# Optimization experiments

Measured on AMD Instinct MI355X. Metric: run time of the kernel, lower is better.

The kernel has to match this reference:

```python
import jax, jax.numpy as jnp
from jax import lax
import numpy as np

A = 9                 # 3 scales x 3 ratios
PRE_NMS_TOPN = 4000
POST_NMS_TOPN = 2000
NMS_THRESH = 0.7
MIN_SIZE = 16.0       # min_size * im_scale (im_info scale = 1)
NEG_INF = -1e9


def generate_anchors(base_size=16, ratios=(0.5, 1.0, 2.0), scales=(8, 16, 32)):
    ratios = np.array(ratios, dtype=np.float64)
    scales = np.array(scales, dtype=np.float64)
    w = h = float(base_size)
    xc = yc = 0.5 * (base_size - 1)
    size = w * h
    ws_r = np.round(np.sqrt(size / ratios))          # [3]
    hs_r = np.round(ws_r * ratios)                   # [3]
    ws = (ws_r[:, None] * scales[None, :]).reshape(-1)   # [9]
    hs = (hs_r[:, None] * scales[None, :]).reshape(-1)   # [9]
    anchors = np.stack([xc - 0.5 * (ws - 1), yc - 0.5 * (hs - 1),
                        xc + 0.5 * (ws - 1), yc + 0.5 * (hs - 1)], axis=1)
    return anchors.astype(np.float32)                # [9,4]


def _conv(x, w, b, padding):
    y = lax.conv_general_dilated(x, w, (1, 1), padding,
                                 dimension_numbers=('NCHW', 'OIHW', 'NCHW'))
    return y + b[None, :, None, None]


def _bbox_transform_inv(anchors, deltas):
    w = anchors[:, 2] - anchors[:, 0] + 1.0
    h = anchors[:, 3] - anchors[:, 1] + 1.0
    cx = anchors[:, 0] + 0.5 * w
    cy = anchors[:, 1] + 0.5 * h
    pcx = deltas[:, 0] * w + cx
    pcy = deltas[:, 1] * h + cy
    pw = jnp.exp(deltas[:, 2]) * w
    ph = jnp.exp(deltas[:, 3]) * h
    return jnp.stack([pcx - 0.5 * pw, pcy - 0.5 * ph,
                      pcx + 0.5 * pw, pcy + 0.5 * ph], axis=1)


def _greedy_nms(boxes, keep_init, thresh):
    # boxes already sorted by descending score; keep_init masks invalid rows
    x1, y1, x2, y2 = boxes[:, 0], boxes[:, 1], boxes[:, 2], boxes[:, 3]
    areas = (x2 - x1 + 1.0) * (y2 - y1 + 1.0)
    xx1 = jnp.maximum(x1[:, None], x1[None, :])
    yy1 = jnp.maximum(y1[:, None], y1[None, :])
    xx2 = jnp.minimum(x2[:, None], x2[None, :])
    yy2 = jnp.minimum(y2[:, None], y2[None, :])
    inter = jnp.maximum(0.0, xx2 - xx1 + 1.0) * jnp.maximum(0.0, yy2 - yy1 + 1.0)
    iou = inter / (areas[:, None] + areas[None, :] - inter)   # [N,N]
    n = boxes.shape[0]
    idx = jnp.arange(n)

    def body(i, keep):
        suppress = keep[i] & (iou[i] > thresh) & (idx > i)
        return keep & ~suppress

    return lax.fori_loop(0, n, body, keep_init)


def reference(im, feats, w_conv, b_conv, w_cls, b_cls, w_reg, b_reg):
    im_h, im_w = im.shape[2], im.shape[3]
    fh, fw = feats.shape[2], feats.shape[3]
    stride = round(im_w / fw)

    # RPN head (classifier)
    hid = jax.nn.relu(_conv(feats, w_conv, b_conv, 'SAME'))
    rpn_map = _conv(hid, w_cls, b_cls, 'SAME')       # [1, 2A, fh, fw]
    rpn_bbox = _conv(hid, w_reg, b_reg, 'SAME')      # [1, 4A, fh, fw]

    # anchor generation: [K*A, 4], shift-major / anchor-minor
    base = jnp.asarray(generate_anchors())
    sx = jnp.arange(fw, dtype=jnp.float32) * stride
    sy = jnp.arange(fh, dtype=jnp.float32) * stride
    sxx, syy = jnp.meshgrid(sx, sy)                  # [fh, fw]
    shifts = jnp.stack([sxx.ravel(), syy.ravel(), sxx.ravel(), syy.ravel()], 1)
    anchors = (base[None, :, :] + shifts[:, None, :]).reshape(-1, 4)

    # predictions, flattened in (h, w, a) order to match anchors
    deltas = rpn_bbox.transpose(0, 2, 3, 1).reshape(-1, 4)
    scores = rpn_map[:, A:, :, :].transpose(0, 2, 3, 1).reshape(-1)

    proposals = _bbox_transform_inv(anchors, deltas)
    # clip_boxes to image
    proposals = jnp.stack([
        jnp.clip(proposals[:, 0], 0.0, im_w - 1.0),
        jnp.clip(proposals[:, 1], 0.0, im_h - 1.0),
        jnp.clip(proposals[:, 2], 0.0, im_w - 1.0),
        jnp.clip(proposals[:, 3], 0.0, im_h - 1.0)], axis=1)

    # filter_boxes (min_size) expressed as a score mask (jit-friendly)
    ws = proposals[:, 2] - proposals[:, 0] + 1.0
    hs = proposals[:, 3] - proposals[:, 1] + 1.0
    valid = (ws >= MIN_SIZE) & (hs >= MIN_SIZE)
    masked_scores = jnp.where(valid, scores, NEG_INF)

    # sort descending, take pre_nms_topN
    order = jnp.argsort(-masked_scores)[:PRE_NMS_TOPN]
    top_boxes = proposals[order]
    top_scores = masked_scores[order]
    keep_init = top_scores > NEG_INF / 2

    keep = _greedy_nms(top_boxes, keep_init, NMS_THRESH)

    # take first post_nms_topN kept (already in score order), padded with zeros
    rank = jnp.cumsum(keep) - 1
    take = keep & (rank < POST_NMS_TOPN)
    dst = jnp.where(take, rank, 0)
    out_boxes = jnp.zeros((POST_NMS_TOPN, 4), dtype=top_boxes.dtype)
    out_boxes = out_boxes.at[dst].add(jnp.where(take[:, None], top_boxes, 0.0))
    out_scores = jnp.zeros((POST_NMS_TOPN, 1), dtype=top_scores.dtype)
    out_scores = out_scores.at[dst].add(jnp.where(take[:, None], top_scores[:, None], 0.0))
    return out_boxes, out_scores


def setup_inputs() -> dict:
    key = jax.random.key(0)
    ks = jax.random.split(key, 8)
    # small weight scale keeps exp(dw) in a sane range, as a trained RPN would
    return {
        'im': jax.random.normal(ks[0], (1, 3, 800, 1216), jnp.float32),
        'feats': jax.random.normal(ks[1], (1, 1024, 50, 76), jnp.float32),
        'w_conv': jax.random.normal(ks[2], (512, 1024, 3, 3), jnp.float32) * 0.001,
        'b_conv': jnp.zeros((512,), jnp.float32),
        'w_cls': jax.random.normal(ks[3], (18, 512, 1, 1), jnp.float32) * 0.01,
        'b_cls': jnp.zeros((18,), jnp.float32),
        'w_reg': jax.random.normal(ks[4], (36, 512, 1, 1), jnp.float32) * 0.01,
        'b_reg': jnp.zeros((36,), jnp.float32),
    }
```

## Files before the change

### kernel.cpp

```cpp
#include <hip/hip_runtime.h>
#include <stdint.h>
#include <math.h>

typedef unsigned long long u64;
typedef unsigned int u32;

#define CIN     1024
#define COUT    512
#define FH      50
#define FW      76
#define QP      80
#define HIDP    4096
#define FPITCH  4160
#define NPOS    3800
#define NA      34200
#define PRE_N   4000
#define POST_N  2000
#define MASKW   63
#define TBN     4032
#define KSLICES 8
#define CPS     128
#define QT      256

#define P0 (3*CIN*FPITCH)
#define P2 (512*48)
#define P3 65536

__device__ __forceinline__ void async16(const float* g, float* l) {
  __builtin_amdgcn_global_load_lds(
      (__attribute__((address_space(1))) void*)(g),
      (__attribute__((address_space(3))) void*)(l), 16, 0, 0);
}

__global__ void k_prep(const float* __restrict__ feats,
                       const float* __restrict__ w_cls, const float* __restrict__ b_cls,
                       const float* __restrict__ w_reg, const float* __restrict__ b_reg,
                       float* __restrict__ fpad3, float* __restrict__ wT, float* __restrict__ bT,
                       u32* __restrict__ hist, u32* __restrict__ ctrl,
                       double4* __restrict__ tb, float* __restrict__ ts) {
  int idx = blockIdx.x * 256 + threadIdx.x;
  if (idx < P0) {
    int tc = idx / (CIN * FPITCH);
    int rem = idx - tc * (CIN * FPITCH);
    int cin = rem / FPITCH;
    int j = rem - cin * FPITCH + tc;
    float v = 0.f;
    if (j < FPITCH) {
      int r = j / QP, u = j - r * QP;
      if (r >= 1 && r <= FH && u >= 1 && u <= FW)
        v = feats[cin * (FH * FW) + (r - 1) * FW + (u - 1)];
    }
    fpad3[idx] = v;
    return;
  }
  idx -= P0;
  if (idx < P2) {
    int c = idx / 48, o = idx - c * 48;
    float v = 0.f;
    if (o < 9) v = w_cls[(size_t)(9 + o) * 512 + c];
    else if (o < 45) v = w_reg[(size_t)(o - 9) * 512 + c];
    wT[idx] = v;
    return;
  }
  idx -= P2;
  if (idx < P3) {
    hist[idx] = 0;
    if (idx < 8) ctrl[idx] = 0;
    if (idx < 48) bT[idx] = (idx < 9) ? b_cls[9 + idx] : (idx < 45 ? b_reg[idx - 9] : 0.f);
    if (idx >= PRE_N && idx < TBN) { tb[idx] = make_double4(0.0, 0.0, 0.0, 0.0); ts[idx] = -1.0e9f; }
  }
}

__global__ void k_wt(const float* __restrict__ w, float* __restrict__ wt) {
  __shared__ float t[64][65];
  int k0 = blockIdx.x * 64, oc0 = blockIdx.y * 64;
  int tx = threadIdx.x & 63, tg = threadIdx.x >> 6;
#pragma unroll
  for (int rr = 0; rr < 16; rr++) {
    int row = tg * 16 + rr;
    t[row][tx] = w[(size_t)(oc0 + row) * 9216 + k0 + tx];
  }
  __syncthreads();
#pragma unroll
  for (int rr = 0; rr < 16; rr++) {
    int kr = tg * 16 + rr;
    wt[(size_t)(k0 + kr) * 512 + oc0 + tx] = t[tx][kr];
  }
}

__global__ __launch_bounds__(256, 4) void k_conv(const float* __restrict__ fpad3,
                                                 const float* __restrict__ wt,
                                                 float* __restrict__ hidp) {
  __shared__ __align__(16) float Bl[2][9][QT];
  const int tid = threadIdx.x;
  const int lane = tid & 63;
  const int wv = __builtin_amdgcn_readfirstlane(tid >> 6);
  const int q0 = blockIdx.x * QT;
  const int ws = (blockIdx.y << 2) + wv;
  const int c0 = blockIdx.z * CPS;

  const int rA = wv;
  const int rB = wv + 4;
  u32 offA = (u32)(rA % 3) * (CIN * FPITCH) + (u32)(rA / 3) * QP + q0 + lane * 4;
  u32 offB = (u32)(rB % 3) * (CIN * FPITCH) + (u32)(rB / 3) * QP + q0 + lane * 4;
  u32 offC = 2u * (CIN * FPITCH) + 2u * QP + q0 + lane * 4;

  float acc32[8][4];
  double acc64[8][4];
#pragma unroll
  for (int i = 0; i < 8; i++)
#pragma unroll
    for (int j = 0; j < 4; j++) { acc32[i][j] = 0.f; acc64[i][j] = 0.0; }

#define STAGE(buf, s)  do {                                                     \
    const float* _b = fpad3 + (size_t)(c0 + (s)) * FPITCH;                      \
    async16(_b + offA, &Bl[buf][rA][0]);                                        \
    async16(_b + offB, &Bl[buf][rB][0]);                                        \
    if (wv == 0) async16(_b + offC, &Bl[buf][8][0]);                            \
  } while (0)

  STAGE(0, 0);

#pragma unroll 1
  for (int s = 0; s < CPS; s++) {
    __syncthreads();
    if (s + 1 < CPS) STAGE((s + 1) & 1, s + 1);
    const float* wp = wt + ((size_t)(c0 + s) * 9 << 9) + (ws << 3);
    const int buf = s & 1;
#pragma unroll
    for (int ks = 0; ks < 9; ks++) {
      float4 b4 = *(const float4*)&Bl[buf][ks][lane * 4];
      const float* w8 = wp + (ks << 9);
#pragma unroll
      for (int i = 0; i < 8; i++) {
        float w = w8[i];
        acc32[i][0] = fmaf(w, b4.x, acc32[i][0]);
        acc32[i][1] = fmaf(w, b4.y, acc32[i][1]);
        acc32[i][2] = fmaf(w, b4.z, acc32[i][2]);
        acc32[i][3] = fmaf(w, b4.w, acc32[i][3]);
      }
    }
    if ((s & 7) == 7) {
#pragma unroll
      for (int i = 0; i < 8; i++)
#pragma unroll
        for (int j = 0; j < 4; j++) { acc64[i][j] += (double)acc32[i][j]; acc32[i][j] = 0.f; }
    }
  }
#undef STAGE

#pragma unroll
  for (int i = 0; i < 8; i++) {
    float4 o;
    o.x = (float)acc64[i][0];
    o.y = (float)acc64[i][1];
    o.z = (float)acc64[i][2];
    o.w = (float)acc64[i][3];
    *(float4*)&hidp[((size_t)(blockIdx.z * COUT + (ws << 3) + i) << 12) + q0 + lane * 4] = o;
  }
}

__global__ void k_reduce(const float* __restrict__ hidp, const float* __restrict__ bconv,
                         float* __restrict__ hid) {
  int idx = blockIdx.x * 256 + threadIdx.x;
  int oc = idx >> 12;
  double s = 0.0;
#pragma unroll
  for (int z = 0; z < KSLICES; z++)
    s += (double)hidp[idx + ((size_t)z << 21)];
  s += (double)bconv[oc];
  hid[idx] = s > 0.0 ? (float)s : 0.f;
}

__global__ __launch_bounds__(256, 8) void k_head(const float* __restrict__ hid,
                                                 const float* __restrict__ wT,
                                                 const float* __restrict__ bT,
                                                 float* __restrict__ scoresb,
                                                 float* __restrict__ deltab) {
  int lane = threadIdx.x & 63;
  int wv = threadIdx.x >> 6;
  int q = blockIdx.x * 64 + lane;
  int og = blockIdx.y * 12 + wv * 3;
  double acc0 = 0.0, acc1 = 0.0, acc2 = 0.0;
#pragma unroll 4
  for (int c = 0; c < 512; c++) {
    double hv = (double)hid[((size_t)c << 12) + q];
    const float* wr = wT + c * 48 + og;
    acc0 += hv * (double)wr[0];
    acc1 += hv * (double)wr[1];
    acc2 += hv * (double)wr[2];
  }
  int y = q / QP, x = q - y * QP;
  if (x < FW && y < FH) {
    int pos = y * FW + x;
    double a[3] = {acc0, acc1, acc2};
#pragma unroll
    for (int j = 0; j < 3; j++) {
      int o = og + j;
      float r = (float)(a[j] + (double)bT[o]);
      if (o < 9)       scoresb[o * NPOS + pos] = r;
      else if (o < 45) deltab[(o - 9) * NPOS + pos] = r;
    }
  }
}

__device__ __constant__ float AW[9] = {184.f, 368.f, 736.f, 128.f, 256.f, 512.f, 88.f, 176.f, 352.f};
__device__ __constant__ float AH[9] = {96.f, 192.f, 384.f, 128.f, 256.f, 512.f, 176.f, 352.f, 704.f};

__global__ void k_prop(const float* __restrict__ scoresb, const float* __restrict__ deltab,
                       double4* __restrict__ boxesd, u64* __restrict__ keys,
                       float* __restrict__ smask, u32* __restrict__ hist,
                       float* __restrict__ dout) {
  int g = blockIdx.x * 256 + threadIdx.x;
  if (g < 10000) dout[g] = 0.f;
  if (g >= NA) return;
  int pos = g / 9, a = g - pos * 9;
  int y = pos / FW, x = pos - y * FW;
  double w = (double)AW[a], h = (double)AH[a];
  double cx = x * 16.0 + 8.0, cy = y * 16.0 + 8.0;
  double d0 = (double)deltab[(4 * a + 0) * NPOS + pos];
  double d1 = (double)deltab[(4 * a + 1) * NPOS + pos];
  double d2 = (double)deltab[(4 * a + 2) * NPOS + pos];
  double d3 = (double)deltab[(4 * a + 3) * NPOS + pos];
  double pcx = d0 * w + cx, pcy = d1 * h + cy;
  double pw = exp(d2) * w, ph = exp(d3) * h;
  double px1 = fmin(fmax(pcx - 0.5 * pw, 0.0), 1215.0);
  double py1 = fmin(fmax(pcy - 0.5 * ph, 0.0), 799.0);
  double px2 = fmin(fmax(pcx + 0.5 * pw, 0.0), 1215.0);
  double py2 = fmin(fmax(pcy + 0.5 * ph, 0.0), 799.0);
  bool valid = (px2 - px1 + 1.0 >= 16.0) && (py2 - py1 + 1.0 >= 16.0);
  float sc = scoresb[a * NPOS + pos];
  float ms = valid ? sc : -1.0e9f;
  boxesd[g] = make_double4(px1, py1, px2, py2);
  smask[g] = ms;
  u32 u = __float_as_uint(ms);
  u = (u >> 31) ? ~u : (u | 0x80000000u);
  keys[g] = ((u64)u << 32) | (u32)(~(u32)g);
  atomicAdd(&hist[u >> 16], 1u);
}

__global__ void k_scan(const u32* __restrict__ hist, u32* __restrict__ ctrl) {
  __shared__ u32 cs[256];
  __shared__ u32 sfx[256];
  int t = threadIdx.x;
  u32 s = 0;
  for (int i = 0; i < 256; i++) s += hist[t * 256 + i];
  cs[t] = s;
  __syncthreads();
  if (t == 0) {
    u32 c = 0;
    for (int i = 255; i >= 0; i--) { sfx[i] = c; c += cs[i]; }
  }
  __syncthreads();
  u32 before = sfx[t];
  u32 c = 0;
  for (int b = 255; b >= 0; b--) {
    u32 hv = hist[t * 256 + b];
    if (before + c < PRE_N && before + c + hv >= PRE_N) {
      ctrl[0] = (u32)(t * 256 + b);
      ctrl[1] = before + c;
    }
    c += hv;
  }
}

__global__ void k_compact(const u64* __restrict__ keys, u32* __restrict__ ctrl,
                          u64* __restrict__ candK, u32* __restrict__ candG) {
  int g = blockIdx.x * 256 + threadIdx.x;
  if (g >= NA) return;
  u32 binB = ctrl[0];
  u64 k = keys[g];
  if ((u32)(k >> 48) >= binB) {
    u32 idx = atomicAdd(&ctrl[2], 1u);
    candK[idx] = k;
    candG[idx] = g;
  }
}

__global__ void k_rank(const u64* __restrict__ candK, const u32* __restrict__ candG,
                       const u32* __restrict__ ctrl, const double4* __restrict__ boxesd,
                       const float* __restrict__ smask, double4* __restrict__ tb,
                       float* __restrict__ ts) {
  __shared__ u64 kk[256];
  u32 m = ctrl[2];
  if (blockIdx.x * 256 >= m) return;
  int i = blockIdx.x * 256 + threadIdx.x;
  u64 my = (i < (int)m) ? candK[i] : 0ULL;
  u32 rank = 0;
  for (u32 base = 0; base < m; base += 256) {
    u32 j = base + threadIdx.x;
    kk[threadIdx.x] = (j < m) ? candK[j] : 0ULL;
    __syncthreads();
    u32 lim = m - base; if (lim > 256) lim = 256;
    for (u32 tt = 0; tt < lim; tt++) rank += (kk[tt] > my) ? 1u : 0u;
    __syncthreads();
  }
  if (i < (int)m && rank < PRE_N) {
    u32 g = candG[i];
    tb[rank] = boxesd[g];
    ts[rank] = smask[g];
  }
}

__global__ void k_mask(const double4* __restrict__ tb, u64* __restrict__ mask) {
  __shared__ double4 bx[64];
  int w = blockIdx.x;
  int i = blockIdx.y * 256 + threadIdx.x;
  if (threadIdx.x < 64) bx[threadIdx.x] = tb[w * 64 + threadIdx.x];
  __syncthreads();
  if (i >= PRE_N) return;
  double4 b = tb[i];
  double ai = (b.z - b.x + 1.0) * (b.w - b.y + 1.0);
  u64 word = 0;
#pragma unroll 8
  for (int j = 0; j < 64; j++) {
    int jg = w * 64 + j;
    double4 cc = bx[j];
    double xx1 = fmax(b.x, cc.x), yy1 = fmax(b.y, cc.y);
    double xx2 = fmin(b.z, cc.z), yy2 = fmin(b.w, cc.w);
    double iw = xx2 - xx1 + 1.0, ih = yy2 - yy1 + 1.0;
    iw = iw > 0.0 ? iw : 0.0; ih = ih > 0.0 ? ih : 0.0;
    double inter = iw * ih;
    double aj = (cc.z - cc.x + 1.0) * (cc.w - cc.y + 1.0);
    bool sup = (jg > i) && (inter > 0.7 * (ai + aj - inter));
    word |= sup ? (1ULL << j) : 0ULL;
  }
  mask[(size_t)i * MASKW + w] = word;
}

__global__ __launch_bounds__(64, 1) void k_nms(const u64* __restrict__ mask,
                                               const float* __restrict__ ts,
                                               const double4* __restrict__ tb,
                                               float* __restrict__ out) {
  int lane = threadIdx.x;
  u64 keep = 0;
  for (int w = 0; w < MASKW; w++) {
    float s = ts[w * 64 + lane];
    u64 b = __ballot(s > -5.0e8f);
    if (lane == w) keep = b;
  }
  for (int c = 0; c < MASKW; c++) {
    u64 cur = __shfl(keep, c);
    u64 D = mask[(size_t)(c * 64 + lane) * MASKW + c];
    for (int j = 0; j < 64; j++) {
      u64 Dj = __shfl(D, j);
      if ((cur >> j) & 1ULL) cur &= ~Dj;
    }
    if (lane == c) keep = cur;
    u64 supp = 0;
#pragma unroll 1
    for (int jb = 0; jb < 64; jb += 16) {
      u64 v[16];
#pragma unroll
      for (int u2 = 0; u2 < 16; u2++)
        v[u2] = (lane < MASKW) ? mask[(size_t)(c * 64 + jb + u2) * MASKW + lane] : 0ULL;
#pragma unroll
      for (int u2 = 0; u2 < 16; u2++)
        if ((cur >> (jb + u2)) & 1ULL) supp |= v[u2];
    }
    keep &= ~supp;
  }
  int pc = __popcll(keep);
  int pre = pc;
#pragma unroll
  for (int off = 1; off < 64; off <<= 1) {
    int v = __shfl_up(pre, off);
    if (lane >= off) pre += v;
  }
  pre -= pc;
#pragma unroll 1
  for (int j = 0; j < 64; j++) {
    if ((keep >> j) & 1ULL) {
      int r = pre + __popcll(keep & ((1ULL << j) - 1ULL));
      if (r < POST_N) {
        int i = lane * 64 + j;
        double4 b = tb[i];
        out[r * 4 + 0] = (float)b.x;
        out[r * 4 + 1] = (float)b.y;
        out[r * 4 + 2] = (float)b.z;
        out[r * 4 + 3] = (float)b.w;
        out[8000 + r] = ts[i];
      }
    }
  }
}

extern "C" void kernel_launch(void* const* d_in, const int* in_sizes, int n_in,
                              void* d_out, int out_size, void* d_ws, size_t ws_size,
                              hipStream_t stream) {
  const float* feats  = (const float*)d_in[1];
  const float* w_conv = (const float*)d_in[2];
  const float* b_conv = (const float*)d_in[3];
  const float* w_cls  = (const float*)d_in[4];
  const float* b_cls  = (const float*)d_in[5];
  const float* w_reg  = (const float*)d_in[6];
  const float* b_reg  = (const float*)d_in[7];
  float* out = (float*)d_out;

  char* p = (char*)d_ws;
  auto carve = [&p](size_t bytes) -> void* {
    void* r = (void*)p;
    p += (bytes + 255) & ~(size_t)255;
    return r;
  };
  float*   fpad3   = (float*)carve(sizeof(float) * (P0 + 512));
  float*   wt      = (float*)carve(sizeof(float) * 9216 * 512);
  float*   wT      = (float*)carve(sizeof(float) * P2);
  float*   bT      = (float*)carve(sizeof(float) * 48);
  float*   hid     = (float*)carve(sizeof(float) * COUT * HIDP);
  float*   hidp    = (float*)carve(sizeof(float) * KSLICES * COUT * HIDP);
  float*   scoresb = (float*)carve(sizeof(float) * 9 * NPOS);
  float*   deltab  = (float*)carve(sizeof(float) * 36 * NPOS);
  double4* boxesd  = (double4*)carve(sizeof(double4) * NA);
  u64*     keys    = (u64*)carve(sizeof(u64) * NA);
  float*   smask   = (float*)carve(sizeof(float) * NA);
  u32*     hist    = (u32*)carve(sizeof(u32) * 65536);
  u32*     ctrl    = (u32*)carve(256);
  u64*     candK   = (u64*)carve(sizeof(u64) * NA);
  u32*     candG   = (u32*)carve(sizeof(u32) * NA);
  double4* tb      = (double4*)carve(sizeof(double4) * TBN);
  float*   ts      = (float*)carve(sizeof(float) * TBN);
  u64*     maskb   = (u64*)carve(sizeof(u64) * (size_t)TBN * MASKW);
  (void)ws_size; (void)in_sizes; (void)n_in; (void)out_size;

  int prep_blocks = (P0 + P2 + P3) / 256;
  k_prep<<<prep_blocks, 256, 0, stream>>>(feats, w_cls, b_cls, w_reg, b_reg,
                                          fpad3, wT, bT, hist, ctrl, tb, ts);
  k_wt<<<dim3(144, 8), 256, 0, stream>>>(w_conv, wt);
  k_conv<<<dim3(16, 16, KSLICES), 256, 0, stream>>>(fpad3, wt, hidp);
  k_reduce<<<8192, 256, 0, stream>>>(hidp, b_conv, hid);
  k_head<<<dim3(64, 4), 256, 0, stream>>>(hid, wT, bT, scoresb, deltab);
  k_prop<<<134, 256, 0, stream>>>(scoresb, deltab, boxesd, keys, smask, hist, out);
  k_scan<<<1, 256, 0, stream>>>(hist, ctrl);
  k_compact<<<134, 256, 0, stream>>>(keys, ctrl, candK, candG);
  k_rank<<<134, 256, 0, stream>>>(candK, candG, ctrl, boxesd, smask, tb, ts);
  k_mask<<<dim3(MASKW, 16), 256, 0, stream>>>(tb, maskb);
  k_nms<<<1, 64, 0, stream>>>(maskb, ts, tb, out);
}
```

Measured before the change: 1.150 ms.

## Fuse pipeline into fewer kernels and stage conv weights through LDS

Merges the weight transpose into the prep kernel and writes a conv-friendly weight layout. The conv kernel now loads its weights asynchronously into LDS alongside the input tiles. Reduce and head are fused into one kernel that keeps the hidden tile in shared memory, and all post-processing stages run as one persistent kernel with software grid barriers. This cuts launch overhead and global round trips, but the grid barrier relies on all 256 blocks being co-resident, and the fused head runs only 64 blocks.

```diff
diff --git a/kernel.cpp b/kernel.cpp
--- a/kernel.cpp
+++ b/kernel.cpp
@@ -25,19 +25,48 @@
 #define P0 (3*CIN*FPITCH)
 #define P2 (512*48)
 #define P3 65536
-
+#define PREP_BLKS ((P0+P2+P3)/256)
+#define WT_BLKS   (144*8)
+
+__device__ __forceinline__ void async4(const float* g, float* l) {
+  __builtin_amdgcn_global_load_lds(
+      (__attribute__((address_space(1))) void*)(g),
+      (__attribute__((address_space(3))) void*)(l), 4, 0, 0);
+}
 __device__ __forceinline__ void async16(const float* g, float* l) {
   __builtin_amdgcn_global_load_lds(
       (__attribute__((address_space(1))) void*)(g),
       (__attribute__((address_space(3))) void*)(l), 16, 0, 0);
 }
 
-__global__ void k_prep(const float* __restrict__ feats,
+__global__ void k_prep(const float* __restrict__ feats, const float* __restrict__ w_conv,
                        const float* __restrict__ w_cls, const float* __restrict__ b_cls,
                        const float* __restrict__ w_reg, const float* __restrict__ b_reg,
-                       float* __restrict__ fpad3, float* __restrict__ wT, float* __restrict__ bT,
+                       float* __restrict__ fpad3, float* __restrict__ wt2,
+                       float* __restrict__ wT, float* __restrict__ bT,
                        u32* __restrict__ hist, u32* __restrict__ ctrl,
                        double4* __restrict__ tb, float* __restrict__ ts) {
+  __shared__ float t[64][65];
+  if (blockIdx.x >= PREP_BLKS) {
+    int bt_ = blockIdx.x - PREP_BLKS;
+    int kx = bt_ % 144, oy = bt_ / 144;
+    int k0 = kx * 64, oc0 = oy * 64;
+    int tx = threadIdx.x & 63, tg = threadIdx.x >> 6;
+#pragma unroll
+    for (int rr = 0; rr < 16; rr++) {
+      int row = tg * 16 + rr;
+      t[row][tx] = w_conv[(size_t)(oc0 + row) * 9216 + k0 + tx];
+    }
+    __syncthreads();
+#pragma unroll
+    for (int rr = 0; rr < 16; rr++) {
+      int kr = tg * 16 + rr;
+      int k = k0 + kr;
+      int c = k / 9, ks = k - c * 9;
+      wt2[(size_t)c * 4608 + (oc0 >> 3) * 72 + (tx >> 3) * 72 + ks * 8 + (tx & 7)] = t[tx][kr];
+    }
+    return;
+  }
   int idx = blockIdx.x * 256 + threadIdx.x;
   if (idx < P0) {
     int tc = idx / (CIN * FPITCH);
@@ -71,27 +100,11 @@
   }
 }
 
-__global__ void k_wt(const float* __restrict__ w, float* __restrict__ wt) {
-  __shared__ float t[64][65];
-  int k0 = blockIdx.x * 64, oc0 = blockIdx.y * 64;
-  int tx = threadIdx.x & 63, tg = threadIdx.x >> 6;
-#pragma unroll
-  for (int rr = 0; rr < 16; rr++) {
-    int row = tg * 16 + rr;
-    t[row][tx] = w[(size_t)(oc0 + row) * 9216 + k0 + tx];
-  }
-  __syncthreads();
-#pragma unroll
-  for (int rr = 0; rr < 16; rr++) {
-    int kr = tg * 16 + rr;
-    wt[(size_t)(k0 + kr) * 512 + oc0 + tx] = t[tx][kr];
-  }
-}
-
 __global__ __launch_bounds__(256, 4) void k_conv(const float* __restrict__ fpad3,
-                                                 const float* __restrict__ wt,
+                                                 const float* __restrict__ wt2,
                                                  float* __restrict__ hidp) {
   __shared__ __align__(16) float Bl[2][9][QT];
+  __shared__ __align__(16) float Wl[2][4][72];
   const int tid = threadIdx.x;
   const int lane = tid & 63;
   const int wv = __builtin_amdgcn_readfirstlane(tid >> 6);
@@ -117,6 +130,9 @@
     async16(_b + offA, &Bl[buf][rA][0]);                                        \
     async16(_b + offB, &Bl[buf][rB][0]);                                        \
     if (wv == 0) async16(_b + offC, &Bl[buf][8][0]);                            \
+    const float* _w = wt2 + ((size_t)(c0 + (s)) * 64 + ws) * 72;                \
+    async4(_w + lane, &Wl[buf][wv][0]);                                         \
+    if (lane < 8) async4(_w + 64 + lane, &Wl[buf][wv][64]);                     \
   } while (0)
 
   STAGE(0, 0);
@@ -125,20 +141,45 @@
   for (int s = 0; s < CPS; s++) {
     __syncthreads();
     if (s + 1 < CPS) STAGE((s + 1) & 1, s + 1);
-    const float* wp = wt + ((size_t)(c0 + s) * 9 << 9) + (ws << 3);
     const int buf = s & 1;
+    const float* wl = &Wl[buf][wv][0];
 #pragma unroll
     for (int ks = 0; ks < 9; ks++) {
       float4 b4 = *(const float4*)&Bl[buf][ks][lane * 4];
-      const float* w8 = wp + (ks << 9);
-#pragma unroll
-      for (int i = 0; i < 8; i++) {
-        float w = w8[i];
-        acc32[i][0] = fmaf(w, b4.x, acc32[i][0]);
-        acc32[i][1] = fmaf(w, b4.y, acc32[i][1]);
-        acc32[i][2] = fmaf(w, b4.z, acc32[i][2]);
-        acc32[i][3] = fmaf(w, b4.w, acc32[i][3]);
-      }
+      float4 wA = *(const float4*)(wl + ks * 8);
+      float4 wB = *(const float4*)(wl + ks * 8 + 4);
+      acc32[0][0] = fmaf(wA.x, b4.x, acc32[0][0]);
+      acc32[0][1] = fmaf(wA.x, b4.y, acc32[0][1]);
+      acc32[0][2] = fmaf(wA.x, b4.z, acc32[0][2]);
+      acc32[0][3] = fmaf(wA.x, b4.w, acc32[0][3]);
+      acc32[1][0] = fmaf(wA.y, b4.x, acc32[1][0]);
+      acc32[1][1] = fmaf(wA.y, b4.y, acc32[1][1]);
+      acc32[1][2] = fmaf(wA.y, b4.z, acc32[1][2]);
+      acc32[1][3] = fmaf(wA.y, b4.w, acc32[1][3]);
+      acc32[2][0] = fmaf(wA.z, b4.x, acc32[2][0]);
+      acc32[2][1] = fmaf(wA.z, b4.y, acc32[2][1]);
+      acc32[2][2] = fmaf(wA.z, b4.z, acc32[2][2]);
+      acc32[2][3] = fmaf(wA.z, b4.w, acc32[2][3]);
+      acc32[3][0] = fmaf(wA.w, b4.x, acc32[3][0]);
+      acc32[3][1] = fmaf(wA.w, b4.y, acc32[3][1]);
+      acc32[3][2] = fmaf(wA.w, b4.z, acc32[3][2]);
+      acc32[3][3] = fmaf(wA.w, b4.w, acc32[3][3]);
+      acc32[4][0] = fmaf(wB.x, b4.x, acc32[4][0]);
+      acc32[4][1] = fmaf(wB.x, b4.y, acc32[4][1]);
+      acc32[4][2] = fmaf(wB.x, b4.z, acc32[4][2]);
+      acc32[4][3] = fmaf(wB.x, b4.w, acc32[4][3]);
+      acc32[5][0] = fmaf(wB.y, b4.x, acc32[5][0]);
+      acc32[5][1] = fmaf(wB.y, b4.y, acc32[5][1]);
+      acc32[5][2] = fmaf(wB.y, b4.z, acc32[5][2]);
+      acc32[5][3] = fmaf(wB.y, b4.w, acc32[5][3]);
+      acc32[6][0] = fmaf(wB.z, b4.x, acc32[6][0]);
+      acc32[6][1] = fmaf(wB.z, b4.y, acc32[6][1]);
+      acc32[6][2] = fmaf(wB.z, b4.z, acc32[6][2]);
+      acc32[6][3] = fmaf(wB.z, b4.w, acc32[6][3]);
+      acc32[7][0] = fmaf(wB.w, b4.x, acc32[7][0]);
+      acc32[7][1] = fmaf(wB.w, b4.y, acc32[7][1]);
+      acc32[7][2] = fmaf(wB.w, b4.z, acc32[7][2]);
+      acc32[7][3] = fmaf(wB.w, b4.w, acc32[7][3]);
     }
     if ((s & 7) == 7) {
 #pragma unroll
@@ -160,44 +201,44 @@
   }
 }
 
-__global__ void k_reduce(const float* __restrict__ hidp, const float* __restrict__ bconv,
-                         float* __restrict__ hid) {
-  int idx = blockIdx.x * 256 + threadIdx.x;
-  int oc = idx >> 12;
-  double s = 0.0;
-#pragma unroll
-  for (int z = 0; z < KSLICES; z++)
-    s += (double)hidp[idx + ((size_t)z << 21)];
-  s += (double)bconv[oc];
-  hid[idx] = s > 0.0 ? (float)s : 0.f;
-}
-
-__global__ __launch_bounds__(256, 8) void k_head(const float* __restrict__ hid,
-                                                 const float* __restrict__ wT,
-                                                 const float* __restrict__ bT,
-                                                 float* __restrict__ scoresb,
-                                                 float* __restrict__ deltab) {
-  int lane = threadIdx.x & 63;
-  int wv = threadIdx.x >> 6;
-  int q = blockIdx.x * 64 + lane;
-  int og = blockIdx.y * 12 + wv * 3;
-  double acc0 = 0.0, acc1 = 0.0, acc2 = 0.0;
+__global__ __launch_bounds__(256, 1) void k_redhead(const float* __restrict__ hidp,
+                                                    const float* __restrict__ bconv,
+                                                    const float* __restrict__ wT,
+                                                    const float* __restrict__ bT,
+                                                    float* __restrict__ scoresb,
+                                                    float* __restrict__ deltab) {
+  __shared__ float hl[512 * 64];
+  const int tid = threadIdx.x, lane = tid & 63, wv = tid >> 6;
+  const int q0 = blockIdx.x * 64;
+  const int q = q0 + lane;
+#pragma unroll 1
+  for (int cc = wv; cc < 512; cc += 4) {
+    double s = 0.0;
+#pragma unroll
+    for (int z = 0; z < KSLICES; z++)
+      s += (double)hidp[(((size_t)z * COUT + cc) << 12) + q0 + lane];
+    s += (double)bconv[cc];
+    hl[cc * 64 + lane] = s > 0.0 ? (float)s : 0.f;
+  }
+  __syncthreads();
+  const int og = wv * 12;
+  double acc[12];
+#pragma unroll
+  for (int j = 0; j < 12; j++) acc[j] = 0.0;
 #pragma unroll 4
   for (int c = 0; c < 512; c++) {
-    double hv = (double)hid[((size_t)c << 12) + q];
+    double hv = (double)hl[c * 64 + lane];
     const float* wr = wT + c * 48 + og;
-    acc0 += hv * (double)wr[0];
-    acc1 += hv * (double)wr[1];
-    acc2 += hv * (double)wr[2];
+#pragma unroll
+    for (int j = 0; j < 12; j++) acc[j] += hv * (double)wr[j];
   }
   int y = q / QP, x = q - y * QP;
   if (x < FW && y < FH) {
     int pos = y * FW + x;
-    double a[3] = {acc0, acc1, acc2};
-#pragma unroll
-    for (int j = 0; j < 3; j++) {
+#pragma unroll
+    for (int j = 0; j < 12; j++) {
       int o = og + j;
-      float r = (float)(a[j] + (double)bT[o]);
+      float r = (float)(acc[j] + (double)bT[o]);
       if (o < 9)       scoresb[o * NPOS + pos] = r;
       else if (o < 45) deltab[(o - 9) * NPOS + pos] = r;
     }
@@ -207,179 +248,203 @@
 __device__ __constant__ float AW[9] = {184.f, 368.f, 736.f, 128.f, 256.f, 512.f, 88.f, 176.f, 352.f};
 __device__ __constant__ float AH[9] = {96.f, 192.f, 384.f, 128.f, 256.f, 512.f, 176.f, 352.f, 704.f};
 
-__global__ void k_prop(const float* __restrict__ scoresb, const float* __restrict__ deltab,
-                       double4* __restrict__ boxesd, u64* __restrict__ keys,
-                       float* __restrict__ smask, u32* __restrict__ hist,
-                       float* __restrict__ dout) {
-  int g = blockIdx.x * 256 + threadIdx.x;
-  if (g < 10000) dout[g] = 0.f;
-  if (g >= NA) return;
-  int pos = g / 9, a = g - pos * 9;
-  int y = pos / FW, x = pos - y * FW;
-  double w = (double)AW[a], h = (double)AH[a];
-  double cx = x * 16.0 + 8.0, cy = y * 16.0 + 8.0;
-  double d0 = (double)deltab[(4 * a + 0) * NPOS + pos];
-  double d1 = (double)deltab[(4 * a + 1) * NPOS + pos];
-  double d2 = (double)deltab[(4 * a + 2) * NPOS + pos];
-  double d3 = (double)deltab[(4 * a + 3) * NPOS + pos];
-  double pcx = d0 * w + cx, pcy = d1 * h + cy;
-  double pw = exp(d2) * w, ph = exp(d3) * h;
-  double px1 = fmin(fmax(pcx - 0.5 * pw, 0.0), 1215.0);
-  double py1 = fmin(fmax(pcy - 0.5 * ph, 0.0), 799.0);
-  double px2 = fmin(fmax(pcx + 0.5 * pw, 0.0), 1215.0);
-  double py2 = fmin(fmax(pcy + 0.5 * ph, 0.0), 799.0);
-  bool valid = (px2 - px1 + 1.0 >= 16.0) && (py2 - py1 + 1.0 >= 16.0);
-  float sc = scoresb[a * NPOS + pos];
-  float ms = valid ? sc : -1.0e9f;
-  boxesd[g] = make_double4(px1, py1, px2, py2);
-  smask[g] = ms;
-  u32 u = __float_as_uint(ms);
-  u = (u >> 31) ? ~u : (u | 0x80000000u);
-  keys[g] = ((u64)u << 32) | (u32)(~(u32)g);
-  atomicAdd(&hist[u >> 16], 1u);
-}
-
-__global__ void k_scan(const u32* __restrict__ hist, u32* __restrict__ ctrl) {
+__device__ __forceinline__ void gbar(u32* cnt, u32 target) {
+  __syncthreads();
+  if (threadIdx.x == 0) {
+    __threadfence();
+    atomicAdd(cnt, 1u);
+    while (atomicAdd(cnt, 0u) < target) __builtin_amdgcn_s_sleep(2);
+  }
+  __syncthreads();
+  __threadfence();
+}
+
+__global__ __launch_bounds__(256, 2) void k_post(const float* __restrict__ scoresb,
+                                                 const float* __restrict__ deltab,
+                                                 double4* __restrict__ boxesd,
+                                                 u64* __restrict__ keys,
+                                                 float* __restrict__ smask,
+                                                 u32* __restrict__ hist,
+                                                 u32* __restrict__ ctrl,
+                                                 u64* __restrict__ candK,
+                                                 u32* __restrict__ candG,
+                                                 double4* __restrict__ tb,
+                                                 float* __restrict__ ts,
+                                                 u64* __restrict__ maskb,
+                                                 float* __restrict__ out) {
   __shared__ u32 cs[256];
   __shared__ u32 sfx[256];
-  int t = threadIdx.x;
-  u32 s = 0;
-  for (int i = 0; i < 256; i++) s += hist[t * 256 + i];
-  cs[t] = s;
-  __syncthreads();
-  if (t == 0) {
+  __shared__ u64 kk[256];
+  __shared__ double4 bx[64];
+  u32* bcnt = &ctrl[7];
+  const int tid = threadIdx.x;
+  int g = blockIdx.x * 256 + tid;
+
+  if (g < 10000) out[g] = 0.f;
+  if (g < NA) {
+    int pos = g / 9, a = g - pos * 9;
+    int y = pos / FW, x = pos - y * FW;
+    double w = (double)AW[a], h = (double)AH[a];
+    double cx = x * 16.0 + 8.0, cy = y * 16.0 + 8.0;
+    double d0 = (double)deltab[(4 * a + 0) * NPOS + pos];
+    double d1 = (double)deltab[(4 * a + 1) * NPOS + pos];
+    double d2 = (double)deltab[(4 * a + 2) * NPOS + pos];
+    double d3 = (double)deltab[(4 * a + 3) * NPOS + pos];
+    double pcx = d0 * w + cx, pcy = d1 * h + cy;
+    double pw = exp(d2) * w, ph = exp(d3) * h;
+    double px1 = fmin(fmax(pcx - 0.5 * pw, 0.0), 1215.0);
+    double py1 = fmin(fmax(pcy - 0.5 * ph, 0.0), 799.0);
+    double px2 = fmin(fmax(pcx + 0.5 * pw, 0.0), 1215.0);
+    double py2 = fmin(fmax(pcy + 0.5 * ph, 0.0), 799.0);
+    bool valid = (px2 - px1 + 1.0 >= 16.0) && (py2 - py1 + 1.0 >= 16.0);
+    float sc = scoresb[a * NPOS + pos];
+    float ms = valid ? sc : -1.0e9f;
+    boxesd[g] = make_double4(px1, py1, px2, py2);
+    smask[g] = ms;
+    u32 u = __float_as_uint(ms);
+    u = (u >> 31) ? ~u : (u | 0x80000000u);
+    keys[g] = ((u64)u << 32) | (u32)(~(u32)g);
+    atomicAdd(&hist[u >> 16], 1u);
+  }
+  gbar(bcnt, 256);
+
+  if (blockIdx.x == 0) {
+    u32 s = 0;
+    for (int i = 0; i < 256; i++) s += hist[tid * 256 + i];
+    cs[tid] = s;
+    __syncthreads();
+    if (tid == 0) {
+      u32 c = 0;
+      for (int i = 255; i >= 0; i--) { sfx[i] = c; c += cs[i]; }
+    }
+    __syncthreads();
+    u32 before = sfx[tid];
     u32 c = 0;
-    for (int i = 255; i >= 0; i--) { sfx[i] = c; c += cs[i]; }
-  }
-  __syncthreads();
-  u32 before = sfx[t];
-  u32 c = 0;
-  for (int b = 255; b >= 0; b--) {
-    u32 hv = hist[t * 256 + b];
-    if (before + c < PRE_N && before + c + hv >= PRE_N) {
-      ctrl[0] = (u32)(t * 256 + b);
-      ctrl[1] = before + c;
-    }
-    c += hv;
-  }
-}
-
-__global__ void k_compact(const u64* __restrict__ keys, u32* __restrict__ ctrl,
-                          u64* __restrict__ candK, u32* __restrict__ candG) {
-  int g = blockIdx.x * 256 + threadIdx.x;
-  if (g >= NA) return;
-  u32 binB = ctrl[0];
-  u64 k = keys[g];
-  if ((u32)(k >> 48) >= binB) {
-    u32 idx = atomicAdd(&ctrl[2], 1u);
-    candK[idx] = k;
-    candG[idx] = g;
-  }
-}
-
-__global__ void k_rank(const u64* __restrict__ candK, const u32* __restrict__ candG,
-                       const u32* __restrict__ ctrl, const double4* __restrict__ boxesd,
-                       const float* __restrict__ smask, double4* __restrict__ tb,
-                       float* __restrict__ ts) {
-  __shared__ u64 kk[256];
-  u32 m = ctrl[2];
-  if (blockIdx.x * 256 >= m) return;
-  int i = blockIdx.x * 256 + threadIdx.x;
-  u64 my = (i < (int)m) ? candK[i] : 0ULL;
-  u32 rank = 0;
-  for (u32 base = 0; base < m; base += 256) {
-    u32 j = base + threadIdx.x;
-    kk[threadIdx.x] = (j < m) ? candK[j] : 0ULL;
-    __syncthreads();
-    u32 lim = m - base; if (lim > 256) lim = 256;
-    for (u32 tt = 0; tt < lim; tt++) rank += (kk[tt] > my) ? 1u : 0u;
-    __syncthreads();
-  }
-  if (i < (int)m && rank < PRE_N) {
-    u32 g = candG[i];
-    tb[rank] = boxesd[g];
-    ts[rank] = smask[g];
-  }
-}
-
-__global__ void k_mask(const double4* __restrict__ tb, u64* __restrict__ mask) {
-  __shared__ double4 bx[64];
-  int w = blockIdx.x;
-  int i = blockIdx.y * 256 + threadIdx.x;
-  if (threadIdx.x < 64) bx[threadIdx.x] = tb[w * 64 + threadIdx.x];
-  __syncthreads();
-  if (i >= PRE_N) return;
-  double4 b = tb[i];
-  double ai = (b.z - b.x + 1.0) * (b.w - b.y + 1.0);
-  u64 word = 0;
+    for (int b = 255; b >= 0; b--) {
+      u32 hv = hist[tid * 256 + b];
+      if (before + c < PRE_N && before + c + hv >= PRE_N) {
+        ctrl[0] = (u32)(tid * 256 + b);
+        ctrl[1] = before + c;
+      }
+      c += hv;
+    }
+  }
+  gbar(bcnt, 512);
+
+  if (g < NA) {
+    u32 binB = ctrl[0];
+    u64 k = keys[g];
+    if ((u32)(k >> 48) >= binB) {
+      u32 idx = atomicAdd(&ctrl[2], 1u);
+      candK[idx] = k;
+      candG[idx] = g;
+    }
+  }
+  gbar(bcnt, 768);
+
+  {
+    u32 m = ctrl[2];
+    if (blockIdx.x * 256 < (int)m) {
+      int i = blockIdx.x * 256 + tid;
+      u64 my = (i < (int)m) ? candK[i] : 0ULL;
+      u32 rank = 0;
+      for (u32 base = 0; base < m; base += 256) {
+        u32 j = base + tid;
+        kk[tid] = (j < m) ? candK[j] : 0ULL;
+        __syncthreads();
+        u32 lim = m - base; if (lim > 256) lim = 256;
+        for (u32 tt = 0; tt < lim; tt++) rank += (kk[tt] > my) ? 1u : 0u;
+        __syncthreads();
+      }
+      if (i < (int)m && rank < PRE_N) {
+        u32 gg = candG[i];
+        tb[rank] = boxesd[gg];
+        ts[rank] = smask[gg];
+      }
+    }
+  }
+  gbar(bcnt, 1024);
+
+#pragma unroll 1
+  for (int u0 = blockIdx.x; u0 < MASKW * 16; u0 += 256) {
+    int w = u0 % MASKW, ib = u0 / MASKW;
+    __syncthreads();
+    if (tid < 64) bx[tid] = tb[w * 64 + tid];
+    __syncthreads();
+    int i = ib * 256 + tid;
+    if (i < PRE_N) {
+      double4 b = tb[i];
+      double ai = (b.z - b.x + 1.0) * (b.w - b.y + 1.0);
+      u64 word = 0;
 #pragma unroll 8
-  for (int j = 0; j < 64; j++) {
-    int jg = w * 64 + j;
-    double4 cc = bx[j];
-    double xx1 = fmax(b.x, cc.x), yy1 = fmax(b.y, cc.y);
-    double xx2 = fmin(b.z, cc.z), yy2 = fmin(b.w, cc.w);
-    double iw = xx2 - xx1 + 1.0, ih = yy2 - yy1 + 1.0;
-    iw = iw > 0.0 ? iw : 0.0; ih = ih > 0.0 ? ih : 0.0;
-    double inter = iw * ih;
-    double aj = (cc.z - cc.x + 1.0) * (cc.w - cc.y + 1.0);
-    bool sup = (jg > i) && (inter > 0.7 * (ai + aj - inter));
-    word |= sup ? (1ULL << j) : 0ULL;
-  }
-  mask[(size_t)i * MASKW + w] = word;
-}
-
-__global__ __launch_bounds__(64, 1) void k_nms(const u64* __restrict__ mask,
-                                               const float* __restrict__ ts,
-                                               const double4* __restrict__ tb,
-                                               float* __restrict__ out) {
-  int lane = threadIdx.x;
-  u64 keep = 0;
-  for (int w = 0; w < MASKW; w++) {
-    float s = ts[w * 64 + lane];
-    u64 b = __ballot(s > -5.0e8f);
-    if (lane == w) keep = b;
-  }
-  for (int c = 0; c < MASKW; c++) {
-    u64 cur = __shfl(keep, c);
-    u64 D = mask[(size_t)(c * 64 + lane) * MASKW + c];
+      for (int j = 0; j < 64; j++) {
+        int jg = w * 64 + j;
+        double4 cc = bx[j];
+        double xx1 = fmax(b.x, cc.x), yy1 = fmax(b.y, cc.y);
+        double xx2 = fmin(b.z, cc.z), yy2 = fmin(b.w, cc.w);
+        double iw = xx2 - xx1 + 1.0, ih = yy2 - yy1 + 1.0;
+        iw = iw > 0.0 ? iw : 0.0; ih = ih > 0.0 ? ih : 0.0;
+        double inter = iw * ih;
+        double aj = (cc.z - cc.x + 1.0) * (cc.w - cc.y + 1.0);
+        bool sup = (jg > i) && (inter > 0.7 * (ai + aj - inter));
+        word |= sup ? (1ULL << j) : 0ULL;
+      }
+      maskb[(size_t)i * MASKW + w] = word;
+    }
+  }
+  gbar(bcnt, 1280);
+  if (blockIdx.x != 0 || tid >= 64) return;
+
+  {
+    int lane = tid;
+    u64 keep = 0;
+    for (int w = 0; w < MASKW; w++) {
+      float s = ts[w * 64 + lane];
+      u64 b = __ballot(s > -5.0e8f);
+      if (lane == w) keep = b;
+    }
+    for (int c = 0; c < MASKW; c++) {
+      u64 cur = __shfl(keep, c);
+      u64 D = maskb[(size_t)(c * 64 + lane) * MASKW + c];
+      for (int j = 0; j < 64; j++) {
+        u64 Dj = __shfl(D, j);
+        if ((cur >> j) & 1ULL) cur &= ~Dj;
+      }
+      if (lane == c) keep = cur;
+      u64 supp = 0;
+#pragma unroll 1
+      for (int jb = 0; jb < 64; jb += 16) {
+        u64 v[16];
+#pragma unroll
+        for (int u2 = 0; u2 < 16; u2++)
+          v[u2] = (lane < MASKW) ? maskb[(size_t)(c * 64 + jb + u2) * MASKW + lane] : 0ULL;
+#pragma unroll
+        for (int u2 = 0; u2 < 16; u2++)
+          if ((cur >> (jb + u2)) & 1ULL) supp |= v[u2];
+      }
+      keep &= ~supp;
+    }
+    int pc = __popcll(keep);
+    int pre = pc;
+#pragma unroll
+    for (int off = 1; off < 64; off <<= 1) {
+      int v = __shfl_up(pre, off);
+      if (lane >= off) pre += v;
+    }
+    pre -= pc;
+#pragma unroll 1
     for (int j = 0; j < 64; j++) {
-      u64 Dj = __shfl(D, j);
-      if ((cur >> j) & 1ULL) cur &= ~Dj;
-    }
-    if (lane == c) keep = cur;
-    u64 supp = 0;
-#pragma unroll 1
-    for (int jb = 0; jb < 64; jb += 16) {
-      u64 v[16];
-#pragma unroll
-      for (int u2 = 0; u2 < 16; u2++)
-        v[u2] = (lane < MASKW) ? mask[(size_t)(c * 64 + jb + u2) * MASKW + lane] : 0ULL;
-#pragma unroll
-      for (int u2 = 0; u2 < 16; u2++)
-        if ((cur >> (jb + u2)) & 1ULL) supp |= v[u2];
-    }
-    keep &= ~supp;
-  }
-  int pc = __popcll(keep);
-  int pre = pc;
-#pragma unroll
-  for (int off = 1; off < 64; off <<= 1) {
-    int v = __shfl_up(pre, off);
-    if (lane >= off) pre += v;
-  }
-  pre -= pc;
-#pragma unroll 1
-  for (int j = 0; j < 64; j++) {
-    if ((keep >> j) & 1ULL) {
-      int r = pre + __popcll(keep & ((1ULL << j) - 1ULL));
-      if (r < POST_N) {
-        int i = lane * 64 + j;
-        double4 b = tb[i];
-        out[r * 4 + 0] = (float)b.x;
-        out[r * 4 + 1] = (float)b.y;
-        out[r * 4 + 2] = (float)b.z;
-        out[r * 4 + 3] = (float)b.w;
-        out[8000 + r] = ts[i];
+      if ((keep >> j) & 1ULL) {
+        int r = pre + __popcll(keep & ((1ULL << j) - 1ULL));
+        if (r < POST_N) {
+          int i = lane * 64 + j;
+          double4 b = tb[i];
+          out[r * 4 + 0] = (float)b.x;
+          out[r * 4 + 1] = (float)b.y;
+          out[r * 4 + 2] = (float)b.z;
+          out[r * 4 + 3] = (float)b.w;
+          out[8000 + r] = ts[i];
+        }
       }
     }
   }
@@ -404,10 +469,9 @@
     return r;
   };
   float*   fpad3   = (float*)carve(sizeof(float) * (P0 + 512));
-  float*   wt      = (float*)carve(sizeof(float) * 9216 * 512);
+  float*   wt2     = (float*)carve(sizeof(float) * 1024 * 4608);
   float*   wT      = (float*)carve(sizeof(float) * P2);
   float*   bT      = (float*)carve(sizeof(float) * 48);
-  float*   hid     = (float*)carve(sizeof(float) * COUT * HIDP);
   float*   hidp    = (float*)carve(sizeof(float) * KSLICES * COUT * HIDP);
   float*   scoresb = (float*)carve(sizeof(float) * 9 * NPOS);
   float*   deltab  = (float*)carve(sizeof(float) * 36 * NPOS);
@@ -423,17 +487,10 @@
   u64*     maskb   = (u64*)carve(sizeof(u64) * (size_t)TBN * MASKW);
   (void)ws_size; (void)in_sizes; (void)n_in; (void)out_size;
 
-  int prep_blocks = (P0 + P2 + P3) / 256;
-  k_prep<<<prep_blocks, 256, 0, stream>>>(feats, w_cls, b_cls, w_reg, b_reg,
-                                          fpad3, wT, bT, hist, ctrl, tb, ts);
-  k_wt<<<dim3(144, 8), 256, 0, stream>>>(w_conv, wt);
-  k_conv<<<dim3(16, 16, KSLICES), 256, 0, stream>>>(fpad3, wt, hidp);
-  k_reduce<<<8192, 256, 0, stream>>>(hidp, b_conv, hid);
-  k_head<<<dim3(64, 4), 256, 0, stream>>>(hid, wT, bT, scoresb, deltab);
-  k_prop<<<134, 256, 0, stream>>>(scoresb, deltab, boxesd, keys, smask, hist, out);
-  k_scan<<<1, 256, 0, stream>>>(hist, ctrl);
-  k_compact<<<134, 256, 0, stream>>>(keys, ctrl, candK, candG);
-  k_rank<<<134, 256, 0, stream>>>(candK, candG, ctrl, boxesd, smask, tb, ts);
-  k_mask<<<dim3(MASKW, 16), 256, 0, stream>>>(tb, maskb);
-  k_nms<<<1, 64, 0, stream>>>(maskb, ts, tb, out);
-}
+  k_prep<<<PREP_BLKS + WT_BLKS, 256, 0, stream>>>(feats, w_conv, w_cls, b_cls, w_reg, b_reg,
+                                                  fpad3, wt2, wT, bT, hist, ctrl, tb, ts);
+  k_conv<<<dim3(16, 16, KSLICES), 256, 0, stream>>>(fpad3, wt2, hidp);
+  k_redhead<<<64, 256, 0, stream>>>(hidp, b_conv, wT, bT, scoresb, deltab);
+  k_post<<<256, 256, 0, stream>>>(scoresb, deltab, boxesd, keys, smask, hist, ctrl,
+                                  candK, candG, tb, ts, maskb, out);
+}
```

Result: slower. 1.738 ms (+51.2%).
